# Optimization experiments

Measured on AMD Instinct MI355X. Metric: run time of the kernel, lower is better.

The kernel has to match this reference:

```python
import jax, jax.numpy as jnp
import numpy as np

V, D, F, M, N = 100000, 300, 768, 64, 512
SURF, CTX, DOC, BODY, H = 4, 50, 100, 200, 5


def setup_inputs() -> dict:
    key = jax.random.key(0)
    ks = jax.random.split(key, 24)
    f32 = jnp.float32
    inp = {
        'embed_table': jax.random.normal(ks[0], (V, D), f32) * 0.02,
        'W_ms': jax.random.normal(ks[1], (F, D, 2), f32) * 0.02,
        'b_ms': jnp.zeros((F,), f32),
        'W_mc': jax.random.normal(ks[2], (F, D, 5), f32) * 0.02,
        'b_mc': jnp.zeros((F,), f32),
        'att_W1': jax.random.normal(ks[3], (2 * D, D), f32) * 0.05,
        'att_b1': jnp.zeros((D,), f32),
        'att_W2': jax.random.normal(ks[4], (D, 1), f32) * 0.05,
        'att_b2': jnp.zeros((1,), f32),
        'll_W': jax.random.normal(ks[5], (7, 1), f32) * 0.3,
        'll_b': jnp.zeros((1,), f32),
        'lamda': jnp.asarray(0.5, f32),
        'mention_ids': jax.random.randint(ks[6], (M, SURF), 0, V, jnp.int32),
        'context_ids': jax.random.randint(ks[7], (M, CTX), 0, V, jnp.int32),
        'doc_ids': jax.random.randint(ks[8], (DOC,), 0, V, jnp.int32),
        'body_ids': jax.random.randint(ks[9], (N, BODY), 0, V, jnp.int32),
        'cand_ids': jax.random.randint(ks[10], (N,), 0, V, jnp.int32),
        'title_vec': jax.random.normal(ks[11], (N, F), f32),
        'bert_doc_vec': jax.random.normal(ks[12], (1, F), f32),
        'hand_features': jax.random.normal(ks[13], (N, 1), f32),
        'm2c_prior': jax.random.uniform(ks[14], (N,), f32),
        'mention_entity': jnp.ones((M, N), f32),
        'entity_entity': (jax.random.uniform(ks[15], (N, N)) < 0.2).astype(f32),
        'entity_sr': jax.random.uniform(ks[16], (N, N), f32),
        'random_k': 5,
    }
    return inp


def _conv_relu_avg(x, W, b):
    # x [B,L,300] -> conv1d(valid) -> relu -> mean over time -> [B,F]
    y = jax.lax.conv_general_dilated(jnp.transpose(x, (0, 2, 1)), W, (1,), 'VALID',
                                     dimension_numbers=('NCH', 'OIH', 'NCH'))
    return jax.nn.relu(y + b[None, :, None]).mean(axis=2)


def _l2n(x, eps=1e-6):
    return x / jnp.maximum(jnp.linalg.norm(x, axis=-1, keepdims=True), eps)


def reference(embed_table, W_ms, b_ms, W_mc, b_mc, att_W1, att_b1, att_W2, att_b2,
              ll_W, ll_b, lamda, mention_ids, context_ids, doc_ids, body_ids, cand_ids,
              title_vec, bert_doc_vec, hand_features, m2c_prior, mention_entity,
              entity_entity, entity_sr, random_k):
    d = embed_table.shape[1]
    hd = d // H
    men_emb = embed_table[mention_ids]           # [M,4,300]
    ctx_emb = embed_table[context_ids]           # [M,50,300]
    doc_emb = embed_table[doc_ids]               # [100,300]
    body_emb = embed_table[body_ids]             # [N,200,300]
    cand_emb = embed_table[cand_ids]             # [N,300]

    ms = _conv_relu_avg(men_emb, W_ms, b_ms)     # [M,768]
    mc = _conv_relu_avg(ctx_emb, W_mc, b_mc)     # [M,768]
    md = bert_doc_vec                            # [1,768]

    tn = _l2n(title_vec)
    cos_st = _l2n(ms) @ tn.T                     # [M,N]
    cos_dt = _l2n(md) @ tn.T                     # [1,N]
    cos_ct = _l2n(mc) @ tn.T                     # [M,N]

    # parameterless 5-head cross attention doc<->body, max over queries
    qh = doc_emb.reshape(doc_emb.shape[0], H, hd)
    kh = body_emb.reshape(body_emb.shape[0], body_emb.shape[1], H, hd)
    sc = jnp.einsum('qhd,nkhd->nhqk', qh, kh) / np.sqrt(hd).astype(np.float32)
    att_db = jnp.einsum('nhqk,nkhd->nqhd', jax.nn.softmax(sc, -1), kh)
    att_db = att_db.reshape(att_db.shape[0], att_db.shape[1], d).max(axis=1)   # [N,300]
    sc2 = jnp.einsum('nkhd,qhd->nhkq', kh, qh) / np.sqrt(hd).astype(np.float32)
    att_bd = jnp.einsum('nhkq,qhd->nkhd', jax.nn.softmax(sc2, -1), qh)
    att_bd = att_bd.reshape(att_bd.shape[0], att_bd.shape[1], d).max(axis=1)   # [N,300]
    comb = jnp.concatenate([att_db, att_bd], axis=-1)                          # [N,600]
    att_score = jax.nn.sigmoid(jax.nn.relu(comb @ att_W1 + att_b1) @ att_W2 + att_b2)[:, 0]  # [N]

    # local context attention ranker: max dot(cand, ctx token) / sqrt(d)
    local_att = jnp.einsum('itd,jd->ijt', ctx_emb, cand_emb).max(-1) / np.sqrt(d).astype(np.float32)  # [M,N]

    m, n = cos_st.shape
    feats = jnp.stack([
        jnp.broadcast_to(hand_features[:, 0][None, :], (m, n)),
        jnp.broadcast_to(m2c_prior[None, :], (m, n)),
        local_att,
        jnp.broadcast_to(att_score[None, :], (m, n)),
        cos_st,
        jnp.broadcast_to(cos_dt, (m, n)),
        cos_ct,
    ], axis=-1)                                   # [M,N,7]
    raw = jnp.einsum('mnf,fo->mn', feats, ll_W) + ll_b[0]

    mask = mention_entity
    cnt = mask.sum(1, keepdims=True)
    mean = (raw * mask).sum(1, keepdims=True) / cnt
    var = (((raw - mean) ** 2) * mask).sum(1, keepdims=True) / (cnt - 1)  # unbiased, torch.std
    z = (raw - mean) / jnp.sqrt(var)
    local_score = z * mask
    sm = jax.nn.softmax(jnp.where(mask > 0, z, -jnp.inf), axis=1) * mask
    zmin = jnp.min(jnp.where(mask > 0, z, jnp.inf), 1, keepdims=True)
    zmax = jnp.max(jnp.where(mask > 0, z, -jnp.inf), 1, keepdims=True)
    u = (z + 1 - zmin) / (zmax - zmin) * mask
    uni = u / u.sum(1, keepdims=True)

    # global score: keep top-3 candidates per mention, row-normalize SR, power-iterate
    top_idx = jax.lax.top_k(sm, 3)[1]                                   # [M,3]
    keep = jnp.zeros((n,), raw.dtype).at[top_idx.reshape(-1)].set(1.0)
    SR = entity_sr * entity_entity * keep[None, :]
    rs = SR.sum(1, keepdims=True)
    SR = jnp.where(jnp.abs(rs) < 1e-6, SR, SR / jnp.where(jnp.abs(rs) < 1e-6, 1.0, rs))
    s = sm.sum(0, keepdims=True)                                        # [1,N]
    fai = s
    for _ in range(int(random_k)):
        fai = (1 - lamda) * (fai @ SR) + lamda * s
    global_score = mention_entity * fai                                 # [M,N]
    return (s, fai, global_score)
```

## Files before the change

### kernel.cpp

```cpp
#include <hip/hip_runtime.h>
#include <math.h>

#define MM 64
#define NN 512
#define DD 300
#define FF 768
#define CTXL 50
#define DOCL 100
#define BODYL 200
#define NHEAD 5
#define HD 60

typedef __attribute__((ext_vector_type(8))) short bf16x8;
typedef __attribute__((ext_vector_type(4))) float f32x4;
#define MFMA16(A,B,C) __builtin_amdgcn_mfma_f32_16x16x32_bf16(A,B,C,0,0,0)

__device__ __forceinline__ ushort f2bf(float f) {
  uint u = __float_as_uint(f);
  uint r = (u + 0x7FFFu + ((u >> 16) & 1u)) >> 16;
  return (ushort)r;
}
__device__ __forceinline__ float bf2f(ushort h) {
  return __uint_as_float(((uint)h) << 16);
}

static constexpr size_t OFF_MS    = 0;
static constexpr size_t OFF_MC    = 49152;
static constexpr size_t OFF_TNORM = 98304;
static constexpr size_t OFF_COSDT = 98816;
static constexpr size_t OFF_CAND  = 99328;
static constexpr size_t OFF_DOC   = 252928;
static constexpr size_t OFF_COMB  = 282928;
static constexpr size_t OFF_ATTS  = 590128;
static constexpr size_t OFF_COSST = 590640;
static constexpr size_t OFF_COSCT = 623408;
static constexpr size_t OFF_LOCATT= 656176;
static constexpr size_t OFF_S     = 688944;
static constexpr size_t OFF_KEEP  = 689456;
static constexpr size_t OFF_INV   = 689968;
static constexpr size_t OFF_FAI_A = 690480;
static constexpr size_t OFF_FAI_B = 690992;
static constexpr size_t OFF_CTXG  = 691504;
static constexpr size_t OFF_WT    = 1689904;

__global__ __launch_bounds__(64) void k_init(
    const float* __restrict__ embed, const float* __restrict__ title,
    const float* __restrict__ bert, const int* __restrict__ cand_ids,
    const int* __restrict__ doc_ids, float* __restrict__ ws) {
  int n = blockIdx.x, t = threadIdx.x;
  float ss = 0.f, dd = 0.f, bb = 0.f;
  for (int j = t; j < FF; j += 64) {
    float tv = title[(size_t)n*FF + j], bv = bert[j];
    ss += tv*tv; dd += tv*bv; bb += bv*bv;
  }
#pragma unroll
  for (int o = 32; o; o >>= 1) {
    ss += __shfl_down(ss, o); dd += __shfl_down(dd, o); bb += __shfl_down(bb, o);
  }
  if (t == 0) {
    float tn = fmaxf(sqrtf(ss), 1e-6f);
    float bn = fmaxf(sqrtf(bb), 1e-6f);
    ws[OFF_TNORM + n] = tn;
    ws[OFF_COSDT + n] = dd / (tn * bn);
  }
  size_t cid = (size_t)cand_ids[n] * DD;
  for (int j = t; j < DD; j += 64) ws[OFF_CAND + (size_t)n*DD + j] = embed[cid + j];
  if (n < DOCL) {
    size_t did = (size_t)doc_ids[n] * DD;
    for (int j = t; j < DD; j += 64) ws[OFF_DOC + (size_t)n*DD + j] = embed[did + j];
  }
  if (n == 0) {
    for (int j = t; j < NN; j += 64) { ws[OFF_S + j] = 0.f; ws[OFF_KEEP + j] = 0.f; }
  }
}

__global__ __launch_bounds__(256) void k_gather(
    const float* __restrict__ embed, const int* __restrict__ context_ids,
    float* __restrict__ ws) {
  int m = blockIdx.x, t = threadIdx.x;
  float* dst = ws + OFF_CTXG + (size_t)m*52*DD;
  for (int i = t; i < 52*DD; i += 256) {
    int r = i / DD, c = i - r*DD;
    dst[i] = (r < CTXL) ? embed[(size_t)context_ids[m*CTXL + r]*DD + c] : 0.f;
  }
}

__global__ __launch_bounds__(256) void k_wt(
    const float* __restrict__ W, float* __restrict__ ws) {
  int kd = blockIdx.x;
  int k = kd / DD, d = kd - k*DD;
  int t = threadIdx.x;
  float* dst = ws + OFF_WT + (size_t)kd*FF;
  for (int f = t; f < FF; f += 256) dst[f] = W[(size_t)f*(DD*5) + d*5 + k];
}

__global__ __launch_bounds__(256) void k_ms(
    const float* __restrict__ embed, const int* __restrict__ mention_ids,
    const float* __restrict__ W, const float* __restrict__ b, float* __restrict__ ws) {
  __shared__ float x[4][DD];
  int m = blockIdx.x, t = threadIdx.x;
  for (int i = t; i < 4*DD; i += 256) {
    int r = i / DD, c = i % DD;
    x[r][c] = embed[(size_t)mention_ids[m*4 + r]*DD + c];
  }
  __syncthreads();
  for (int f = t; f < FF; f += 256) {
    const float* w = W + (size_t)f * (DD*2);
    float bb = b[f];
    float acc = 0.f;
#pragma unroll
    for (int tt = 0; tt < 3; ++tt) {
      float y = bb;
      for (int d = 0; d < DD; ++d) {
        float2 wv = *(const float2*)&w[d*2];
        y += wv.x * x[tt][d] + wv.y * x[tt+1][d];
      }
      acc += fmaxf(y, 0.f);
    }
    ws[OFF_MS + (size_t)m*FF + f] = acc * (1.f/3.f);
  }
}

__global__ __launch_bounds__(256) void k_mc_gemm(
    const float* __restrict__ b_mc, float* __restrict__ ws) {
  __shared__ float As[50][49];
  __shared__ float Bs[50][128];
  int m = blockIdx.x, f0 = blockIdx.y * 128, t = threadIdx.x;
  int tr = t >> 4, tc = t & 15;
  const float* ctxm = ws + OFF_CTXG + (size_t)m*52*DD;
  const float4* wt4 = (const float4*)(ws + OFF_WT);
  float acc[3][8];
#pragma unroll
  for (int r = 0; r < 3; ++r)
#pragma unroll
    for (int j = 0; j < 8; ++j) acc[r][j] = 0.f;

  for (int chunk = 0; chunk < 30; ++chunk) {
    int k = chunk / 6, dc = (chunk - k*6) * 50;
    for (int i = t; i < 48*50; i += 256) {
      int row = i / 50, kj = i - row*50;
      As[kj][row] = ctxm[(row + k)*DD + dc + kj];
    }
    for (int i = t; i < 1600; i += 256) {
      int kj = i >> 5, fq = i & 31;
      *(float4*)&Bs[kj][fq*4] = wt4[((size_t)(k*DD + dc + kj)*FF + f0 + fq*4) >> 2];
    }
    __syncthreads();
#pragma unroll 2
    for (int kj = 0; kj < 50; ++kj) {
      float a0 = As[kj][tr], a1 = As[kj][tr+16], a2 = As[kj][tr+32];
      float4 b0 = *(const float4*)&Bs[kj][tc*8];
      float4 b1 = *(const float4*)&Bs[kj][tc*8+4];
      float bb[8] = {b0.x,b0.y,b0.z,b0.w,b1.x,b1.y,b1.z,b1.w};
#pragma unroll
      for (int j = 0; j < 8; ++j) {
        acc[0][j] += a0*bb[j]; acc[1][j] += a1*bb[j]; acc[2][j] += a2*bb[j];
      }
    }
    __syncthreads();
  }
  float bv[8], p[8];
#pragma unroll
  for (int j = 0; j < 8; ++j) { bv[j] = b_mc[f0 + tc*8 + j]; p[j] = 0.f; }
#pragma unroll
  for (int rr = 0; rr < 3; ++rr) {
    int row = tr + 16*rr;
    if (row < 46) {
#pragma unroll
      for (int j = 0; j < 8; ++j) p[j] += fmaxf(acc[rr][j] + bv[j], 0.f);
    }
  }
  float* red = &Bs[0][0];
#pragma unroll
  for (int j = 0; j < 8; ++j) red[tr*128 + tc*8 + j] = p[j];
  __syncthreads();
  if (t < 128) {
    float s = 0.f;
#pragma unroll
    for (int i = 0; i < 16; ++i) s += red[i*128 + t];
    ws[OFF_MC + (size_t)m*FF + f0 + t] = s * (1.f/46.f);
  }
}

__global__ __launch_bounds__(256) void k_cos(
    const float* __restrict__ title, float* __restrict__ ws) {
  __shared__ float a[FF], bv_[FF];
  __shared__ float redA[4], redB[4];
  int m = blockIdx.x, t = threadIdx.x;
  float pa = 0.f, pb = 0.f;
  for (int j = t; j < FF; j += 256) {
    float v = ws[OFF_MS + (size_t)m*FF + j]; a[j] = v; pa += v*v;
    float u = ws[OFF_MC + (size_t)m*FF + j]; bv_[j] = u; pb += u*u;
  }
#pragma unroll
  for (int o = 32; o; o >>= 1) { pa += __shfl_down(pa, o); pb += __shfl_down(pb, o); }
  if ((t & 63) == 0) { redA[t>>6] = pa; redB[t>>6] = pb; }
  __syncthreads();
  float na = fmaxf(sqrtf(redA[0]+redA[1]+redA[2]+redA[3]), 1e-6f);
  float nb = fmaxf(sqrtf(redB[0]+redB[1]+redB[2]+redB[3]), 1e-6f);
  float ia = 1.f / na, ib = 1.f / nb;
  for (int n = t; n < NN; n += 256) {
    const float4* tr = (const float4*)(title + (size_t)n*FF);
    float ds = 0.f, dc = 0.f;
    for (int j = 0; j < FF/4; ++j) {
      float4 tv = tr[j];
      float4 av = *(const float4*)&a[j*4];
      float4 bw = *(const float4*)&bv_[j*4];
      ds += av.x*tv.x + av.y*tv.y + av.z*tv.z + av.w*tv.w;
      dc += bw.x*tv.x + bw.y*tv.y + bw.z*tv.z + bw.w*tv.w;
    }
    float it = 1.f / ws[OFF_TNORM + n];
    ws[OFF_COSST + (size_t)m*NN + n] = ds * ia * it;
    ws[OFF_COSCT + (size_t)m*NN + n] = dc * ib * it;
  }
}

__global__ __launch_bounds__(256) void k_att(
    const float* __restrict__ embed, const int* __restrict__ body_ids,
    float* __restrict__ ws) {
  __shared__ __align__(16) ushort qhB[112*64];
  __shared__ __align__(16) ushort qhT[64*128];
  __shared__ __align__(16) ushort khBc[32*64];
  __shared__ __align__(16) ushort khTc[64*48];
  __shared__ __align__(16) ushort XA[112*48];
  __shared__ __align__(16) ushort XT[32*128];
  __shared__ float rs_acc[112];
  __shared__ float cs_c[32];
  __shared__ float csqL[64];
  __shared__ float cskL[64];

  const float SCALE = 0.1290994448735806f;
  int n = blockIdx.x, h = blockIdx.y, t = threadIdx.x;
  int w = t >> 6, l = t & 63;
  int l15 = l & 15, l4 = l >> 4;
  const float* doc = ws + OFF_DOC;

  if (t < 112) rs_acc[t] = 0.f;
  else if (t < 176) cskL[t-112] = 0.f;
  if (t < 64) {
    int kk = t >> 1, ls = 14 + (t & 1);
    int ps = ls ^ (kk & 7);
    uint4 z = {0,0,0,0};
    *(uint4*)&XT[kk*128 + ps*8] = z;
  }

  for (int u = t; u < 112*8; u += 256) {
    int q = u >> 3, j8 = u & 7;
    uint pk[4] = {0,0,0,0};
    if (q < 100) {
      const float* src = doc + q*DD + h*HD;
#pragma unroll
      for (int i = 0; i < 8; ++i) {
        int j = j8*8 + i;
        float v = (j < HD) ? src[j] : 0.f;
        pk[i>>1] |= ((uint)f2bf(v)) << ((i & 1) * 16);
      }
    }
    int slot = j8 ^ (q & 7);
    *(uint4*)&qhB[q*64 + slot*8] = make_uint4(pk[0], pk[1], pk[2], pk[3]);
  }
  for (int u = t; u < 64*16; u += 256) {
    int d = u >> 4, q8 = u & 15;
    uint pk[4] = {0,0,0,0};
    if (d < HD) {
#pragma unroll
      for (int i = 0; i < 8; ++i) {
        int q = q8*8 + i;
        float v = (q < 100) ? doc[q*DD + h*HD + d] : 0.f;
        pk[i>>1] |= ((uint)f2bf(v)) << ((i & 1) * 16);
      }
    }
    int slot = q8 ^ (d & 7);
    *(uint4*)&qhT[d*128 + slot*8] = make_uint4(pk[0], pk[1], pk[2], pk[3]);
  }
  __syncthreads();
  if (t < 64) {
    int d = t;
    float s = 0.f;
    for (int ls = 0; ls < 13; ++ls) {
      int ps = ls ^ (d & 7);
      const ushort* p = &qhT[d*128 + ps*8];
#pragma unroll
      for (int i = 0; i < 8; ++i) {
        int q = ls*8 + i;
        if (q < 100) s += bf2f(p[i]);
      }
    }
    csqL[t] = s;
  }
  __syncthreads();
  float csq_r = csqL[16*w + l15];

  f32x4 Cdb[7];
#pragma unroll
  for (int i = 0; i < 7; ++i) Cdb[i] = (f32x4){0.f,0.f,0.f,0.f};
  float bdmx = -1e30f;

  const int* bids = body_ids + n*BODYL;

  for (int c = 0; c < 7; ++c) {
    int k0 = c * 32;
    {
      int kk = t >> 3, j8 = t & 7;
      int kg = k0 + kk;
      uint pk[4] = {0,0,0,0};
      if (kg < BODYL) {
        const float* src = embed + (size_t)bids[kg]*DD + h*HD;
#pragma unroll
        for (int i = 0; i < 8; ++i) {
          int j = j8*8 + i;
          float v = (j < HD) ? src[j] : 0.f;
          pk[i>>1] |= ((uint)f2bf(v)) << ((i & 1) * 16);
        }
      }
      int slot = j8 ^ (kk & 7);
      *(uint4*)&khBc[kk*64 + slot*8] = make_uint4(pk[0], pk[1], pk[2], pk[3]);
    }
    {
      int d = t >> 2, kk8 = t & 3;
      uint pk[4] = {0,0,0,0};
      if (d < HD) {
#pragma unroll
        for (int i = 0; i < 8; ++i) {
          int kg = k0 + kk8*8 + i;
          float v = (kg < BODYL) ? embed[(size_t)bids[kg]*DD + h*HD + d] : 0.f;
          pk[i>>1] |= ((uint)f2bf(v)) << ((i & 1) * 16);
        }
      }
      *(uint4*)&khTc[d*48 + kk8*8] = make_uint4(pk[0], pk[1], pk[2], pk[3]);
    }
    __syncthreads();

    for (int task = w; task < 14; task += 4) {
      int mt = task / 7, nt = task - mt*7;
      int krow = 16*mt + l15;
      int qrow = 16*nt + l15;
      f32x4 acc = {0.f,0.f,0.f,0.f};
#pragma unroll
      for (int js = 0; js < 2; ++js) {
        bf16x8 a = *(const bf16x8*)&khBc[krow*64 + ((js*4 + l4) ^ (krow & 7))*8];
        bf16x8 b = *(const bf16x8*)&qhB[qrow*64 + ((js*4 + l4) ^ (qrow & 7))*8];
        acc = MFMA16(a, b, acc);
      }
      int q = qrow;
      int kkb = 16*mt + 4*l4;
      ushort xs[4];
#pragma unroll
      for (int r = 0; r < 4; ++r) {
        int kg = k0 + kkb + r;
        float x = (q < 100 && kg < BODYL) ? (__expf(acc[r]*SCALE) - 1.f) : 0.f;
        xs[r] = f2bf(x);
      }
      uint2 wv = make_uint2((uint)xs[0] | ((uint)xs[1] << 16),
                            (uint)xs[2] | ((uint)xs[3] << 16));
      *(uint2*)&XA[q*48 + kkb] = wv;
#pragma unroll
      for (int r = 0; r < 4; ++r) {
        int kk = kkb + r;
        XT[kk*128 + (((q >> 3) ^ (kk & 7))*8) + (q & 7)] = xs[r];
      }
    }
    __syncthreads();

    if (t < 112) {
      float s = 0.f;
      const uint4* p = (const uint4*)&XA[t*48];
#pragma unroll
      for (int b4 = 0; b4 < 4; ++b4) {
        uint4 v = p[b4];
        uint vv[4] = {v.x, v.y, v.z, v.w};
#pragma unroll
        for (int i = 0; i < 4; ++i) {
          s += bf2f((ushort)(vv[i] & 0xFFFF)) + bf2f((ushort)(vv[i] >> 16));
        }
      }
      rs_acc[t] += s;
    } else if (t < 144) {
      int kk = t - 112;
      float s = 0.f;
      for (int ls = 0; ls < 14; ++ls) {
        int ps = ls ^ (kk & 7);
        const uint4* p = (const uint4*)&XT[kk*128 + ps*8];
        uint4 v = *p;
        uint vv[4] = {v.x, v.y, v.z, v.w};
#pragma unroll
        for (int i = 0; i < 4; ++i) {
          s += bf2f((ushort)(vv[i] & 0xFFFF)) + bf2f((ushort)(vv[i] >> 16));
        }
      }
      cs_c[kk] = 100.f + s;
    } else if (t < 208) {
      int d = t - 144;
      float s = 0.f;
      const uint4* p = (const uint4*)&khTc[d*48];
#pragma unroll
      for (int b4 = 0; b4 < 4; ++b4) {
        uint4 v = p[b4];
        uint vv[4] = {v.x, v.y, v.z, v.w};
#pragma unroll
        for (int i = 0; i < 4; ++i) {
          s += bf2f((ushort)(vv[i] & 0xFFFF)) + bf2f((ushort)(vv[i] >> 16));
        }
      }
      cskL[d] += s;
    }
    __syncthreads();

    {
      int d = 16*w + l15;
      bf16x8 bfr = *(const bf16x8*)&khTc[d*48 + l4*8];
#pragma unroll
      for (int mt2 = 0; mt2 < 7; ++mt2) {
        int q = 16*mt2 + l15;
        bf16x8 afr = *(const bf16x8*)&XA[q*48 + l4*8];
        Cdb[mt2] = MFMA16(afr, bfr, Cdb[mt2]);
      }
    }
    {
      int d = 16*w + l15;
#pragma unroll
      for (int kt = 0; kt < 2; ++kt) {
        int kk = 16*kt + l15;
        f32x4 acc3 = {0.f,0.f,0.f,0.f};
#pragma unroll
        for (int qs = 0; qs < 4; ++qs) {
          bf16x8 afr = *(const bf16x8*)&XT[kk*128 + ((qs*4 + l4) ^ (kk & 7))*8];
          bf16x8 bfr = *(const bf16x8*)&qhT[d*128 + ((qs*4 + l4) ^ (d & 7))*8];
          acc3 = MFMA16(afr, bfr, acc3);
        }
#pragma unroll
        for (int r = 0; r < 4; ++r) {
          int kkr = 16*kt + 4*l4 + r;
          int kg = k0 + kkr;
          if (kg < BODYL) {
            float v = (csq_r + acc3[r]) / cs_c[kkr];
            bdmx = fmaxf(bdmx, v);
          }
        }
      }
    }
    __syncthreads();
  }

  float csk_r = cskL[16*w + l15];
  float dbmx = -1e30f;
#pragma unroll
  for (int mt2 = 0; mt2 < 7; ++mt2) {
#pragma unroll
    for (int r = 0; r < 4; ++r) {
      int q = 16*mt2 + 4*l4 + r;
      if (q < 100) {
        float v = (csk_r + Cdb[mt2][r]) / (200.f + rs_acc[q]);
        dbmx = fmaxf(dbmx, v);
      }
    }
  }
  dbmx = fmaxf(dbmx, __shfl_xor(dbmx, 16));
  dbmx = fmaxf(dbmx, __shfl_xor(dbmx, 32));
  bdmx = fmaxf(bdmx, __shfl_xor(bdmx, 16));
  bdmx = fmaxf(bdmx, __shfl_xor(bdmx, 32));
  int d = 16*w + l15;
  if (l4 == 0 && d < HD) {
    ws[OFF_COMB + (size_t)n*600 + h*HD + d] = dbmx;
    ws[OFF_COMB + (size_t)n*600 + 300 + h*HD + d] = bdmx;
  }
}

__global__ __launch_bounds__(256) void k_local(
    float* __restrict__ ws) {
  __shared__ __align__(16) float x[CTXL][304];
  __shared__ float red[2][128];
  int m = blockIdx.x, nc = blockIdx.y, t = threadIdx.x;
  const float* ctxm = ws + OFF_CTXG + (size_t)m*52*DD;
  for (int i = t; i < CTXL*DD; i += 256) {
    int r = i / DD, c = i % DD;
    x[r][c] = ctxm[i];
  }
  __syncthreads();
  int nl = t & 127, half = t >> 7;
  int n = nc*128 + nl;
  const float4* cr = (const float4*)(ws + OFF_CAND + (size_t)n*DD);
  float acc[25];
#pragma unroll
  for (int i = 0; i < 25; ++i) acc[i] = 0.f;
  for (int d4 = 0; d4 < 75; ++d4) {
    float4 cv = cr[d4];
#pragma unroll
    for (int i = 0; i < 25; ++i) {
      float4 xv = *(const float4*)&x[half*25 + i][d4*4];
      acc[i] += xv.x*cv.x + xv.y*cv.y + xv.z*cv.z + xv.w*cv.w;
    }
  }
  float mx = -1e30f;
#pragma unroll
  for (int i = 0; i < 25; ++i) mx = fmaxf(mx, acc[i]);
  red[half][nl] = mx;
  __syncthreads();
  if (t < 128) {
    float v = fmaxf(red[0][t], red[1][t]) * 0.05773502691896258f;
    ws[OFF_LOCATT + (size_t)m*NN + nc*128 + t] = v;
  }
}

__global__ __launch_bounds__(256) void k_mlp(
    const float* __restrict__ W1, const float* __restrict__ b1,
    const float* __restrict__ W2, const float* __restrict__ b2,
    float* __restrict__ ws) {
  __shared__ float comb8[8][600];
  __shared__ float acc8[8];
  int b = blockIdx.x, t = threadIdx.x;
  int n0 = b*8;
  for (int i = t; i < 8*600; i += 256)
    comb8[i/600][i%600] = ws[OFF_COMB + (size_t)(n0 + i/600)*600 + (i%600)];
  if (t < 8) acc8[t] = 0.f;
  __syncthreads();
  float psum[8];
#pragma unroll
  for (int nn2 = 0; nn2 < 8; ++nn2) psum[nn2] = 0.f;
  for (int j = t; j < 300; j += 256) {
    float hh[8];
#pragma unroll
    for (int nn2 = 0; nn2 < 8; ++nn2) hh[nn2] = b1[j];
    for (int i = 0; i < 600; ++i) {
      float w = W1[(size_t)i*300 + j];
#pragma unroll
      for (int nn2 = 0; nn2 < 8; ++nn2) hh[nn2] += comb8[nn2][i]*w;
    }
    float w2 = W2[j];
#pragma unroll
    for (int nn2 = 0; nn2 < 8; ++nn2) psum[nn2] += fmaxf(hh[nn2], 0.f)*w2;
  }
#pragma unroll
  for (int nn2 = 0; nn2 < 8; ++nn2) atomicAdd(&acc8[nn2], psum[nn2]);
  __syncthreads();
  if (t < 8) {
    float v = acc8[t] + b2[0];
    ws[OFF_ATTS + n0 + t] = 1.f / (1.f + __expf(-v));
  }
}

__device__ __forceinline__ float bsum512(float v, float* red) {
  int t = threadIdx.x;
#pragma unroll
  for (int o = 32; o; o >>= 1) v += __shfl_down(v, o);
  __syncthreads();
  if ((t & 63) == 0) red[t>>6] = v;
  __syncthreads();
  float s = 0.f;
#pragma unroll
  for (int i = 0; i < 8; ++i) s += red[i];
  return s;
}
__device__ __forceinline__ float bmax512(float v, float* red) {
  int t = threadIdx.x;
#pragma unroll
  for (int o = 32; o; o >>= 1) v = fmaxf(v, __shfl_down(v, o));
  __syncthreads();
  if ((t & 63) == 0) red[t>>6] = v;
  __syncthreads();
  float s = -INFINITY;
#pragma unroll
  for (int i = 0; i < 8; ++i) s = fmaxf(s, red[i]);
  return s;
}

__global__ __launch_bounds__(512) void k_score(
    const float* __restrict__ hand, const float* __restrict__ m2c,
    const float* __restrict__ llW, const float* __restrict__ llb,
    const float* __restrict__ me, float* __restrict__ ws) {
  __shared__ float red[8];
  __shared__ float rv[512];
  __shared__ int ri[512];
  int m = blockIdx.x, t = threadIdx.x;
  float mask = me[(size_t)m*NN + t];
  float raw = llW[0]*hand[t] + llW[1]*m2c[t] + llW[2]*ws[OFF_LOCATT + (size_t)m*NN + t]
            + llW[3]*ws[OFF_ATTS + t] + llW[4]*ws[OFF_COSST + (size_t)m*NN + t]
            + llW[5]*ws[OFF_COSDT + t] + llW[6]*ws[OFF_COSCT + (size_t)m*NN + t] + llb[0];
  float cnt = bsum512(mask, red);
  float mean = bsum512(raw*mask, red) / cnt;
  float dv = raw - mean;
  float var = bsum512(dv*dv*mask, red) / (cnt - 1.f);
  float z = dv / sqrtf(var);
  float zm = (mask > 0.f) ? z : -INFINITY;
  float mx = bmax512(zm, red);
  float e = (mask > 0.f) ? __expf(zm - mx) : 0.f;
  float ssum = bsum512(e, red);
  float sm = e / ssum * mask;
  atomicAdd(&ws[OFF_S + t], sm);
  bool excl = false;
  for (int r = 0; r < 3; ++r) {
    rv[t] = excl ? -INFINITY : zm;
    ri[t] = t;
    __syncthreads();
    for (int off = 256; off; off >>= 1) {
      if (t < off) {
        float bb = rv[t+off]; int ib = ri[t+off];
        if (bb > rv[t] || (bb == rv[t] && ib < ri[t])) { rv[t] = bb; ri[t] = ib; }
      }
      __syncthreads();
    }
    int widx = ri[0];
    __syncthreads();
    if (t == 0) ws[OFF_KEEP + widx] = 1.f;
    if (t == widx) excl = true;
  }
}

__global__ __launch_bounds__(512) void k_grs(
    const float* __restrict__ esr, const float* __restrict__ eee,
    float* __restrict__ ws) {
  __shared__ float keep_l[NN];
  int b = blockIdx.x, t = threadIdx.x;
  keep_l[t] = ws[OFF_KEEP + t];
  __syncthreads();
  int lane = t & 63, w = t >> 6;
  int r = b*8 + w;
  float p = 0.f;
  for (int j = lane; j < NN; j += 64)
    p += esr[(size_t)r*NN + j] * eee[(size_t)r*NN + j] * keep_l[j];
#pragma unroll
  for (int o = 32; o; o >>= 1) p += __shfl_down(p, o);
  if (lane == 0) {
    ws[OFF_INV + r] = (fabsf(p) < 1e-6f) ? 1.f : 1.f/p;
    ws[OFF_FAI_A + r] = ws[OFF_S + r];
  }
}

__global__ __launch_bounds__(512) void k_giter(
    const float* __restrict__ esr, const float* __restrict__ eee,
    const float* __restrict__ lamda, const int* __restrict__ rk,
    const float* __restrict__ fin, float* __restrict__ fout,
    const float* __restrict__ wsro, int it) {
  int b = blockIdx.x, t = threadIdx.x;
  int K = rk[0];
  if (it >= K) {
    if (t < 8) fout[b*8 + t] = fin[b*8 + t];
    return;
  }
  __shared__ float g[NN];
  __shared__ float red[8][65];
  g[t] = fin[t] * wsro[OFF_INV + t];
  __syncthreads();
  float lam = lamda[0];
  int jl = t & 7, ig = t >> 3;
  int j = b*8 + jl;
  float p = 0.f;
  for (int i = ig; i < NN; i += 64)
    p += g[i] * esr[(size_t)i*NN + j] * eee[(size_t)i*NN + j];
  red[jl][ig] = p;
  __syncthreads();
  if (t < 8) {
    float acc = 0.f;
    for (int i = 0; i < 64; ++i) acc += red[t][i];
    int jj = b*8 + t;
    fout[jj] = (1.f - lam) * wsro[OFF_KEEP + jj] * acc + lam * wsro[OFF_S + jj];
  }
}

__global__ __launch_bounds__(512) void k_gout(
    const float* __restrict__ me, const float* __restrict__ ws, float* __restrict__ out) {
  int m = blockIdx.x, t = threadIdx.x;
  float fai = ws[OFF_FAI_A + t];
  if (m == 0) { out[t] = ws[OFF_S + t]; out[NN + t] = fai; }
  out[2*NN + (size_t)m*NN + t] = me[(size_t)m*NN + t] * fai;
}

extern "C" void kernel_launch(void* const* d_in, const int* in_sizes, int n_in,
                              void* d_out, int out_size, void* d_ws, size_t ws_size,
                              hipStream_t stream) {
  const float* embed   = (const float*)d_in[0];
  const float* W_ms    = (const float*)d_in[1];
  const float* b_ms    = (const float*)d_in[2];
  const float* W_mc    = (const float*)d_in[3];
  const float* b_mc    = (const float*)d_in[4];
  const float* att_W1  = (const float*)d_in[5];
  const float* att_b1  = (const float*)d_in[6];
  const float* att_W2  = (const float*)d_in[7];
  const float* att_b2  = (const float*)d_in[8];
  const float* ll_W    = (const float*)d_in[9];
  const float* ll_b    = (const float*)d_in[10];
  const float* lamda   = (const float*)d_in[11];
  const int* mention_ids = (const int*)d_in[12];
  const int* context_ids = (const int*)d_in[13];
  const int* doc_ids     = (const int*)d_in[14];
  const int* body_ids    = (const int*)d_in[15];
  const int* cand_ids    = (const int*)d_in[16];
  const float* title   = (const float*)d_in[17];
  const float* bert    = (const float*)d_in[18];
  const float* hand    = (const float*)d_in[19];
  const float* m2c     = (const float*)d_in[20];
  const float* me      = (const float*)d_in[21];
  const float* eee     = (const float*)d_in[22];
  const float* esr     = (const float*)d_in[23];
  const int* rk        = (const int*)d_in[24];
  float* ws  = (float*)d_ws;
  float* out = (float*)d_out;

  hipLaunchKernelGGL(k_init, dim3(NN), dim3(64), 0, stream, embed, title, bert, cand_ids, doc_ids, ws);
  hipLaunchKernelGGL(k_gather, dim3(MM), dim3(256), 0, stream, embed, context_ids, ws);
  hipLaunchKernelGGL(k_wt, dim3(1500), dim3(256), 0, stream, W_mc, ws);
  hipLaunchKernelGGL(k_ms, dim3(MM), dim3(256), 0, stream, embed, mention_ids, W_ms, b_ms, ws);
  hipLaunchKernelGGL(k_mc_gemm, dim3(MM, 6), dim3(256), 0, stream, b_mc, ws);
  hipLaunchKernelGGL(k_cos, dim3(MM), dim3(256), 0, stream, title, ws);
  hipLaunchKernelGGL(k_att, dim3(NN, NHEAD), dim3(256), 0, stream, embed, body_ids, ws);
  hipLaunchKernelGGL(k_local, dim3(MM, 4), dim3(256), 0, stream, ws);
  hipLaunchKernelGGL(k_mlp, dim3(64), dim3(256), 0, stream, att_W1, att_b1, att_W2, att_b2, ws);
  hipLaunchKernelGGL(k_score, dim3(MM), dim3(512), 0, stream, hand, m2c, ll_W, ll_b, me, ws);
  hipLaunchKernelGGL(k_grs, dim3(64), dim3(512), 0, stream, esr, eee, ws);
  float* fa = ws + OFF_FAI_A;
  float* fb = ws + OFF_FAI_B;
  for (int it = 0; it < 8; ++it) {
    hipLaunchKernelGGL(k_giter, dim3(64), dim3(512), 0, stream, esr, eee, lamda, rk,
                       (it & 1) ? fb : fa, (it & 1) ? fa : fb, ws, it);
  }
  hipLaunchKernelGGL(k_gout, dim3(MM), dim3(512), 0, stream, me, ws, out);
}
```

Measured before the change: 1.054 ms.

## Hoist doc bf16 prep, stage body in LDS once, MFMA sums, pretransposed SR

Doc head tiles are converted to bf16 once per head in a new kernel instead of in each of 2560 attention blocks. All 200 body rows now go into LDS up front, and row and column sums come from MFMA ones-columns instead of scalar reductions, which removes the per-chunk gather and the extra barrier. The normalized, keep-masked SR matrix is precomputed transposed so each power iteration reads one contiguous row per output. The mc GEMM tile also shrinks to 64 columns to launch more blocks. The cost is extra workspace and launches, plus a larger LDS footprint in the attention kernel that may lower occupancy.

Measured after the change: 994.7 us. 1.06x faster.

```diff
diff --git a/kernel.cpp b/kernel.cpp
--- a/kernel.cpp
+++ b/kernel.cpp
@@ -42,6 +42,10 @@
 static constexpr size_t OFF_FAI_B = 690992;
 static constexpr size_t OFF_CTXG  = 691504;
 static constexpr size_t OFF_WT    = 1689904;
+static constexpr size_t OFF_DOCB  = 2841904;
+static constexpr size_t OFF_DOCT  = 2859824;
+static constexpr size_t OFF_CSQ   = 2880304;
+static constexpr size_t OFF_SRNT  = 2880624;
 
 __global__ __launch_bounds__(64) void k_init(
     const float* __restrict__ embed, const float* __restrict__ title,
@@ -74,6 +78,46 @@
   }
 }
 
+__global__ __launch_bounds__(256) void k_doc(float* __restrict__ ws) {
+  int h = blockIdx.x, t = threadIdx.x;
+  const float* doc = ws + OFF_DOC;
+  ushort* docB = (ushort*)(ws + OFF_DOCB) + h*112*64;
+  ushort* docT = (ushort*)(ws + OFF_DOCT) + h*64*128;
+  for (int u = t; u < 112*8; u += 256) {
+    int q = u >> 3, j8 = u & 7;
+    uint pk[4] = {0,0,0,0};
+    if (q < DOCL) {
+#pragma unroll
+      for (int i = 0; i < 8; ++i) {
+        int j = j8*8 + i;
+        float v = (j < HD) ? doc[q*DD + h*HD + j] : 0.f;
+        pk[i>>1] |= ((uint)f2bf(v)) << ((i & 1) * 16);
+      }
+    }
+    *(uint4*)&docB[q*64 + j8*8] = make_uint4(pk[0],pk[1],pk[2],pk[3]);
+  }
+  for (int u = t; u < 64*16; u += 256) {
+    int d = u >> 4, q8 = u & 15;
+    uint pk[4] = {0,0,0,0};
+#pragma unroll
+    for (int i = 0; i < 8; ++i) {
+      int q = q8*8 + i;
+      float v = 0.f;
+      if (q < DOCL) {
+        if (d < HD) v = doc[q*DD + h*HD + d];
+        else if (d == HD) v = 1.f;
+      }
+      pk[i>>1] |= ((uint)f2bf(v)) << ((i & 1) * 16);
+    }
+    *(uint4*)&docT[d*128 + q8*8] = make_uint4(pk[0],pk[1],pk[2],pk[3]);
+  }
+  if (t < 64) {
+    float s = 0.f;
+    if (t < HD) for (int q = 0; q < DOCL; ++q) s += bf2f(f2bf(doc[q*DD + h*HD + t]));
+    ws[OFF_CSQ + h*64 + t] = s;
+  }
+}
+
 __global__ __launch_bounds__(256) void k_gather(
     const float* __restrict__ embed, const int* __restrict__ context_ids,
     float* __restrict__ ws) {
@@ -124,16 +168,16 @@
 __global__ __launch_bounds__(256) void k_mc_gemm(
     const float* __restrict__ b_mc, float* __restrict__ ws) {
   __shared__ float As[50][49];
-  __shared__ float Bs[50][128];
-  int m = blockIdx.x, f0 = blockIdx.y * 128, t = threadIdx.x;
+  __shared__ float Bs[50][64];
+  int m = blockIdx.x, f0 = blockIdx.y * 64, t = threadIdx.x;
   int tr = t >> 4, tc = t & 15;
   const float* ctxm = ws + OFF_CTXG + (size_t)m*52*DD;
   const float4* wt4 = (const float4*)(ws + OFF_WT);
-  float acc[3][8];
+  float acc[3][4];
 #pragma unroll
   for (int r = 0; r < 3; ++r)
 #pragma unroll
-    for (int j = 0; j < 8; ++j) acc[r][j] = 0.f;
+    for (int j = 0; j < 4; ++j) acc[r][j] = 0.f;
 
   for (int chunk = 0; chunk < 30; ++chunk) {
     int k = chunk / 6, dc = (chunk - k*6) * 50;
@@ -141,43 +185,42 @@
       int row = i / 50, kj = i - row*50;
       As[kj][row] = ctxm[(row + k)*DD + dc + kj];
     }
-    for (int i = t; i < 1600; i += 256) {
-      int kj = i >> 5, fq = i & 31;
+    for (int i = t; i < 800; i += 256) {
+      int kj = i >> 4, fq = i & 15;
       *(float4*)&Bs[kj][fq*4] = wt4[((size_t)(k*DD + dc + kj)*FF + f0 + fq*4) >> 2];
     }
     __syncthreads();
 #pragma unroll 2
     for (int kj = 0; kj < 50; ++kj) {
       float a0 = As[kj][tr], a1 = As[kj][tr+16], a2 = As[kj][tr+32];
-      float4 b0 = *(const float4*)&Bs[kj][tc*8];
-      float4 b1 = *(const float4*)&Bs[kj][tc*8+4];
-      float bb[8] = {b0.x,b0.y,b0.z,b0.w,b1.x,b1.y,b1.z,b1.w};
-#pragma unroll
-      for (int j = 0; j < 8; ++j) {
+      float4 b0 = *(const float4*)&Bs[kj][tc*4];
+      float bb[4] = {b0.x,b0.y,b0.z,b0.w};
+#pragma unroll
+      for (int j = 0; j < 4; ++j) {
         acc[0][j] += a0*bb[j]; acc[1][j] += a1*bb[j]; acc[2][j] += a2*bb[j];
       }
     }
     __syncthreads();
   }
-  float bv[8], p[8];
-#pragma unroll
-  for (int j = 0; j < 8; ++j) { bv[j] = b_mc[f0 + tc*8 + j]; p[j] = 0.f; }
+  float bv[4], p[4];
+#pragma unroll
+  for (int j = 0; j < 4; ++j) { bv[j] = b_mc[f0 + tc*4 + j]; p[j] = 0.f; }
 #pragma unroll
   for (int rr = 0; rr < 3; ++rr) {
     int row = tr + 16*rr;
     if (row < 46) {
 #pragma unroll
-      for (int j = 0; j < 8; ++j) p[j] += fmaxf(acc[rr][j] + bv[j], 0.f);
-    }
-  }
-  float* red = &Bs[0][0];
-#pragma unroll
-  for (int j = 0; j < 8; ++j) red[tr*128 + tc*8 + j] = p[j];
-  __syncthreads();
-  if (t < 128) {
+      for (int j = 0; j < 4; ++j) p[j] += fmaxf(acc[rr][j] + bv[j], 0.f);
+    }
+  }
+  float* red = &As[0][0];
+#pragma unroll
+  for (int j = 0; j < 4; ++j) red[tr*64 + tc*4 + j] = p[j];
+  __syncthreads();
+  if (t < 64) {
     float s = 0.f;
 #pragma unroll
-    for (int i = 0; i < 16; ++i) s += red[i*128 + t];
+    for (int i = 0; i < 16; ++i) s += red[i*64 + t];
     ws[OFF_MC + (size_t)m*FF + f0 + t] = s * (1.f/46.f);
   }
 }
@@ -218,239 +261,168 @@
 __global__ __launch_bounds__(256) void k_att(
     const float* __restrict__ embed, const int* __restrict__ body_ids,
     float* __restrict__ ws) {
-  __shared__ __align__(16) ushort qhB[112*64];
-  __shared__ __align__(16) ushort qhT[64*128];
-  __shared__ __align__(16) ushort khBc[32*64];
-  __shared__ __align__(16) ushort khTc[64*48];
-  __shared__ __align__(16) ushort XA[112*48];
+  __shared__ __align__(16) ushort khB[224*64];
+  __shared__ __align__(16) ushort khT[64*232];
+  __shared__ __align__(16) ushort XA[112*56];
   __shared__ __align__(16) ushort XT[32*128];
-  __shared__ float rs_acc[112];
+  __shared__ float rs_l[112];
   __shared__ float cs_c[32];
-  __shared__ float csqL[64];
-  __shared__ float cskL[64];
 
   const float SCALE = 0.1290994448735806f;
   int n = blockIdx.x, h = blockIdx.y, t = threadIdx.x;
   int w = t >> 6, l = t & 63;
   int l15 = l & 15, l4 = l >> 4;
-  const float* doc = ws + OFF_DOC;
-
-  if (t < 112) rs_acc[t] = 0.f;
-  else if (t < 176) cskL[t-112] = 0.f;
-  if (t < 64) {
-    int kk = t >> 1, ls = 14 + (t & 1);
-    int ps = ls ^ (kk & 7);
-    uint4 z = {0,0,0,0};
-    *(uint4*)&XT[kk*128 + ps*8] = z;
-  }
-
-  for (int u = t; u < 112*8; u += 256) {
-    int q = u >> 3, j8 = u & 7;
+  const int* bids = body_ids + n*BODYL;
+  const ushort* docB = (const ushort*)(ws + OFF_DOCB) + h*112*64;
+  const ushort* docT = (const ushort*)(ws + OFF_DOCT) + h*64*128;
+  int dcol = 16*w + l15;
+  float csq_r = ws[OFF_CSQ + h*64 + dcol];
+
+  for (int u = t; u < 224*8; u += 256) {
+    int k = u >> 3, j8 = u & 7;
     uint pk[4] = {0,0,0,0};
-    if (q < 100) {
-      const float* src = doc + q*DD + h*HD;
-#pragma unroll
-      for (int i = 0; i < 8; ++i) {
-        int j = j8*8 + i;
-        float v = (j < HD) ? src[j] : 0.f;
-        pk[i>>1] |= ((uint)f2bf(v)) << ((i & 1) * 16);
-      }
-    }
-    int slot = j8 ^ (q & 7);
-    *(uint4*)&qhB[q*64 + slot*8] = make_uint4(pk[0], pk[1], pk[2], pk[3]);
-  }
-  for (int u = t; u < 64*16; u += 256) {
-    int d = u >> 4, q8 = u & 15;
-    uint pk[4] = {0,0,0,0};
-    if (d < HD) {
-#pragma unroll
-      for (int i = 0; i < 8; ++i) {
-        int q = q8*8 + i;
-        float v = (q < 100) ? doc[q*DD + h*HD + d] : 0.f;
-        pk[i>>1] |= ((uint)f2bf(v)) << ((i & 1) * 16);
-      }
-    }
-    int slot = q8 ^ (d & 7);
-    *(uint4*)&qhT[d*128 + slot*8] = make_uint4(pk[0], pk[1], pk[2], pk[3]);
-  }
-  __syncthreads();
-  if (t < 64) {
-    int d = t;
-    float s = 0.f;
-    for (int ls = 0; ls < 13; ++ls) {
-      int ps = ls ^ (d & 7);
-      const ushort* p = &qhT[d*128 + ps*8];
-#pragma unroll
-      for (int i = 0; i < 8; ++i) {
-        int q = ls*8 + i;
-        if (q < 100) s += bf2f(p[i]);
-      }
-    }
-    csqL[t] = s;
-  }
-  __syncthreads();
-  float csq_r = csqL[16*w + l15];
+    if (k < BODYL) {
+      const float* src = embed + (size_t)bids[k]*DD + h*HD;
+      float4 v0 = *(const float4*)&src[j8*8];
+      float4 v1 = {0.f,0.f,0.f,0.f};
+      if (j8 < 7) v1 = *(const float4*)&src[j8*8+4];
+      pk[0] = (uint)f2bf(v0.x) | ((uint)f2bf(v0.y) << 16);
+      pk[1] = (uint)f2bf(v0.z) | ((uint)f2bf(v0.w) << 16);
+      pk[2] = (uint)f2bf(v1.x) | ((uint)f2bf(v1.y) << 16);
+      pk[3] = (uint)f2bf(v1.z) | ((uint)f2bf(v1.w) << 16);
+    }
+    *(uint4*)&khB[k*64 + (j8 ^ (k & 7))*8] = make_uint4(pk[0],pk[1],pk[2],pk[3]);
+  }
+  for (int u = t; u < 512; u += 256) {
+    int kk = u >> 4, q = 112 + (u & 15);
+    XT[kk*128 + ((q >> 3) ^ (kk & 7))*8 + (q & 7)] = 0;
+  }
+  __syncthreads();
+  for (int v = t; v < 232*64; v += 256) {
+    int d = v & 63, k = v >> 6;
+    ushort val = 0;
+    if (k < BODYL) {
+      if (d < HD) val = khB[k*64 + ((d >> 3) ^ (k & 7))*8 + (d & 7)];
+      else if (d == HD) val = 0x3F80;
+    }
+    khT[d*232 + k] = val;
+  }
+  __syncthreads();
 
   f32x4 Cdb[7];
 #pragma unroll
   for (int i = 0; i < 7; ++i) Cdb[i] = (f32x4){0.f,0.f,0.f,0.f};
-  float bdmx = -1e30f;
-
-  const int* bids = body_ids + n*BODYL;
+  float bdmx = -1e30f, dbmx = -1e30f;
+
+  bf16x8 bfrT[4];
+#pragma unroll
+  for (int qs = 0; qs < 4; ++qs)
+    bfrT[qs] = *(const bf16x8*)&docT[dcol*128 + qs*32 + l4*8];
 
   for (int c = 0; c < 7; ++c) {
-    int k0 = c * 32;
+    int k0 = c*32;
+    for (int task = w; task < 14; task += 4) {
+      int mt = (task >= 7) ? 1 : 0;
+      int nt = task - mt*7;
+      int krow = k0 + 16*mt + l15;
+      int qrow = 16*nt + l15;
+      bf16x8 ka0 = *(const bf16x8*)&khB[krow*64 + ((0 + l4) ^ (krow & 7))*8];
+      bf16x8 ka1 = *(const bf16x8*)&khB[krow*64 + ((4 + l4) ^ (krow & 7))*8];
+      bf16x8 qa0 = *(const bf16x8*)&docB[qrow*64 + l4*8];
+      bf16x8 qa1 = *(const bf16x8*)&docB[qrow*64 + 32 + l4*8];
+      f32x4 d1 = (f32x4){0.f,0.f,0.f,0.f}, d1b = (f32x4){0.f,0.f,0.f,0.f};
+      d1  = MFMA16(ka0, qa0, d1);  d1  = MFMA16(ka1, qa1, d1);
+      d1b = MFMA16(qa0, ka0, d1b); d1b = MFMA16(qa1, ka1, d1b);
+      {
+        int kkb = 16*mt + 4*l4;
+        ushort xs[4];
+#pragma unroll
+        for (int r = 0; r < 4; ++r) {
+          int kg = k0 + kkb + r;
+          float x = 0.f;
+          if (qrow < DOCL) { if (kg < BODYL) x = __expf(d1[r]*SCALE) - 1.f; }
+          else if (qrow == DOCL) { if (kg < BODYL) x = 1.f; }
+          xs[r] = f2bf(x);
+        }
+        uint2 wv = make_uint2((uint)xs[0] | ((uint)xs[1] << 16),
+                              (uint)xs[2] | ((uint)xs[3] << 16));
+        *(uint2*)&XA[qrow*56 + kkb] = wv;
+      }
+      {
+        int kk = 16*mt + l15;
+        int kg = k0 + kk;
+        int q0 = 16*nt + 4*l4;
+        ushort xs[4];
+#pragma unroll
+        for (int r = 0; r < 4; ++r) {
+          int q = q0 + r;
+          float x = (q < DOCL && kg < BODYL) ? (__expf(d1b[r]*SCALE) - 1.f) : 0.f;
+          xs[r] = f2bf(x);
+        }
+        uint2 wv = make_uint2((uint)xs[0] | ((uint)xs[1] << 16),
+                              (uint)xs[2] | ((uint)xs[3] << 16));
+        *(uint2*)&XT[kk*128 + ((q0 >> 3) ^ (kk & 7))*8 + (q0 & 7)] = wv;
+      }
+    }
+    __syncthreads();
     {
-      int kk = t >> 3, j8 = t & 7;
-      int kg = k0 + kk;
-      uint pk[4] = {0,0,0,0};
-      if (kg < BODYL) {
-        const float* src = embed + (size_t)bids[kg]*DD + h*HD;
-#pragma unroll
-        for (int i = 0; i < 8; ++i) {
-          int j = j8*8 + i;
-          float v = (j < HD) ? src[j] : 0.f;
-          pk[i>>1] |= ((uint)f2bf(v)) << ((i & 1) * 16);
+      bf16x8 bfr = *(const bf16x8*)&khT[dcol*232 + k0 + l4*8];
+#pragma unroll
+      for (int mt2 = 0; mt2 < 7; ++mt2) {
+        bf16x8 afr = *(const bf16x8*)&XA[(16*mt2 + l15)*56 + l4*8];
+        Cdb[mt2] = MFMA16(afr, bfr, Cdb[mt2]);
+      }
+    }
+    f32x4 a3[2];
+#pragma unroll
+    for (int kt = 0; kt < 2; ++kt) {
+      int kkl = 16*kt + l15;
+      f32x4 acc = (f32x4){0.f,0.f,0.f,0.f};
+#pragma unroll
+      for (int qs = 0; qs < 4; ++qs) {
+        bf16x8 afr = *(const bf16x8*)&XT[kkl*128 + ((qs*4 + l4) ^ (kkl & 7))*8];
+        acc = MFMA16(afr, bfrT[qs], acc);
+      }
+      a3[kt] = acc;
+    }
+    if (w == 3 && l15 == 12) {
+#pragma unroll
+      for (int kt = 0; kt < 2; ++kt)
+#pragma unroll
+        for (int r = 0; r < 4; ++r)
+          cs_c[16*kt + 4*l4 + r] = 100.f + a3[kt][r];
+    }
+    __syncthreads();
+#pragma unroll
+    for (int kt = 0; kt < 2; ++kt) {
+#pragma unroll
+      for (int r = 0; r < 4; ++r) {
+        int kk = 16*kt + 4*l4 + r;
+        if (k0 + kk < BODYL) {
+          float v = (csq_r + a3[kt][r]) / cs_c[kk];
+          bdmx = fmaxf(bdmx, v);
         }
       }
-      int slot = j8 ^ (kk & 7);
-      *(uint4*)&khBc[kk*64 + slot*8] = make_uint4(pk[0], pk[1], pk[2], pk[3]);
-    }
-    {
-      int d = t >> 2, kk8 = t & 3;
-      uint pk[4] = {0,0,0,0};
-      if (d < HD) {
-#pragma unroll
-        for (int i = 0; i < 8; ++i) {
-          int kg = k0 + kk8*8 + i;
-          float v = (kg < BODYL) ? embed[(size_t)bids[kg]*DD + h*HD + d] : 0.f;
-          pk[i>>1] |= ((uint)f2bf(v)) << ((i & 1) * 16);
-        }
-      }
-      *(uint4*)&khTc[d*48 + kk8*8] = make_uint4(pk[0], pk[1], pk[2], pk[3]);
     }
     __syncthreads();
-
-    for (int task = w; task < 14; task += 4) {
-      int mt = task / 7, nt = task - mt*7;
-      int krow = 16*mt + l15;
-      int qrow = 16*nt + l15;
-      f32x4 acc = {0.f,0.f,0.f,0.f};
-#pragma unroll
-      for (int js = 0; js < 2; ++js) {
-        bf16x8 a = *(const bf16x8*)&khBc[krow*64 + ((js*4 + l4) ^ (krow & 7))*8];
-        bf16x8 b = *(const bf16x8*)&qhB[qrow*64 + ((js*4 + l4) ^ (qrow & 7))*8];
-        acc = MFMA16(a, b, acc);
-      }
-      int q = qrow;
-      int kkb = 16*mt + 4*l4;
-      ushort xs[4];
-#pragma unroll
-      for (int r = 0; r < 4; ++r) {
-        int kg = k0 + kkb + r;
-        float x = (q < 100 && kg < BODYL) ? (__expf(acc[r]*SCALE) - 1.f) : 0.f;
-        xs[r] = f2bf(x);
-      }
-      uint2 wv = make_uint2((uint)xs[0] | ((uint)xs[1] << 16),
-                            (uint)xs[2] | ((uint)xs[3] << 16));
-      *(uint2*)&XA[q*48 + kkb] = wv;
-#pragma unroll
-      for (int r = 0; r < 4; ++r) {
-        int kk = kkb + r;
-        XT[kk*128 + (((q >> 3) ^ (kk & 7))*8) + (q & 7)] = xs[r];
-      }
-    }
-    __syncthreads();
-
-    if (t < 112) {
-      float s = 0.f;
-      const uint4* p = (const uint4*)&XA[t*48];
-#pragma unroll
-      for (int b4 = 0; b4 < 4; ++b4) {
-        uint4 v = p[b4];
-        uint vv[4] = {v.x, v.y, v.z, v.w};
-#pragma unroll
-        for (int i = 0; i < 4; ++i) {
-          s += bf2f((ushort)(vv[i] & 0xFFFF)) + bf2f((ushort)(vv[i] >> 16));
-        }
-      }
-      rs_acc[t] += s;
-    } else if (t < 144) {
-      int kk = t - 112;
-      float s = 0.f;
-      for (int ls = 0; ls < 14; ++ls) {
-        int ps = ls ^ (kk & 7);
-        const uint4* p = (const uint4*)&XT[kk*128 + ps*8];
-        uint4 v = *p;
-        uint vv[4] = {v.x, v.y, v.z, v.w};
-#pragma unroll
-        for (int i = 0; i < 4; ++i) {
-          s += bf2f((ushort)(vv[i] & 0xFFFF)) + bf2f((ushort)(vv[i] >> 16));
-        }
-      }
-      cs_c[kk] = 100.f + s;
-    } else if (t < 208) {
-      int d = t - 144;
-      float s = 0.f;
-      const uint4* p = (const uint4*)&khTc[d*48];
-#pragma unroll
-      for (int b4 = 0; b4 < 4; ++b4) {
-        uint4 v = p[b4];
-        uint vv[4] = {v.x, v.y, v.z, v.w};
-#pragma unroll
-        for (int i = 0; i < 4; ++i) {
-          s += bf2f((ushort)(vv[i] & 0xFFFF)) + bf2f((ushort)(vv[i] >> 16));
-        }
-      }
-      cskL[d] += s;
-    }
-    __syncthreads();
-
-    {
-      int d = 16*w + l15;
-      bf16x8 bfr = *(const bf16x8*)&khTc[d*48 + l4*8];
-#pragma unroll
-      for (int mt2 = 0; mt2 < 7; ++mt2) {
-        int q = 16*mt2 + l15;
-        bf16x8 afr = *(const bf16x8*)&XA[q*48 + l4*8];
-        Cdb[mt2] = MFMA16(afr, bfr, Cdb[mt2]);
-      }
-    }
-    {
-      int d = 16*w + l15;
-#pragma unroll
-      for (int kt = 0; kt < 2; ++kt) {
-        int kk = 16*kt + l15;
-        f32x4 acc3 = {0.f,0.f,0.f,0.f};
-#pragma unroll
-        for (int qs = 0; qs < 4; ++qs) {
-          bf16x8 afr = *(const bf16x8*)&XT[kk*128 + ((qs*4 + l4) ^ (kk & 7))*8];
-          bf16x8 bfr = *(const bf16x8*)&qhT[d*128 + ((qs*4 + l4) ^ (d & 7))*8];
-          acc3 = MFMA16(afr, bfr, acc3);
-        }
-#pragma unroll
-        for (int r = 0; r < 4; ++r) {
-          int kkr = 16*kt + 4*l4 + r;
-          int kg = k0 + kkr;
-          if (kg < BODYL) {
-            float v = (csq_r + acc3[r]) / cs_c[kkr];
-            bdmx = fmaxf(bdmx, v);
-          }
-        }
-      }
-    }
-    __syncthreads();
-  }
-
-  float csk_r = cskL[16*w + l15];
-  float dbmx = -1e30f;
+  }
+
+  if (w == 3 && l15 == 12) {
+#pragma unroll
+    for (int mt2 = 0; mt2 < 7; ++mt2)
+#pragma unroll
+      for (int r = 0; r < 4; ++r)
+        rs_l[16*mt2 + 4*l4 + r] = Cdb[mt2][r];
+  }
+  float csk_r = __shfl(Cdb[6][0], 16 + l15);
+  __syncthreads();
 #pragma unroll
   for (int mt2 = 0; mt2 < 7; ++mt2) {
 #pragma unroll
     for (int r = 0; r < 4; ++r) {
       int q = 16*mt2 + 4*l4 + r;
-      if (q < 100) {
-        float v = (csk_r + Cdb[mt2][r]) / (200.f + rs_acc[q]);
+      if (q < DOCL) {
+        float v = (csk_r + Cdb[mt2][r]) / (200.f + rs_l[q]);
         dbmx = fmaxf(dbmx, v);
       }
     }
@@ -459,10 +431,9 @@
   dbmx = fmaxf(dbmx, __shfl_xor(dbmx, 32));
   bdmx = fmaxf(bdmx, __shfl_xor(bdmx, 16));
   bdmx = fmaxf(bdmx, __shfl_xor(bdmx, 32));
-  int d = 16*w + l15;
-  if (l4 == 0 && d < HD) {
-    ws[OFF_COMB + (size_t)n*600 + h*HD + d] = dbmx;
-    ws[OFF_COMB + (size_t)n*600 + 300 + h*HD + d] = bdmx;
+  if (l4 == 0 && dcol < HD) {
+    ws[OFF_COMB + (size_t)n*600 + h*HD + dcol] = dbmx;
+    ws[OFF_COMB + (size_t)n*600 + 300 + h*HD + dcol] = bdmx;
   }
 }
 
@@ -626,34 +597,32 @@
   }
 }
 
-__global__ __launch_bounds__(512) void k_giter(
+__global__ __launch_bounds__(256) void k_srt(
     const float* __restrict__ esr, const float* __restrict__ eee,
+    float* __restrict__ ws) {
+  int j = blockIdx.x, t = threadIdx.x;
+  float kj = ws[OFF_KEEP + j];
+  float* dst = ws + OFF_SRNT + (size_t)j*NN;
+  for (int i = t; i < NN; i += 256)
+    dst[i] = esr[(size_t)i*NN + j] * eee[(size_t)i*NN + j] * kj * ws[OFF_INV + i];
+}
+
+__global__ __launch_bounds__(256) void k_giter(
     const float* __restrict__ lamda, const int* __restrict__ rk,
     const float* __restrict__ fin, float* __restrict__ fout,
     const float* __restrict__ wsro, int it) {
-  int b = blockIdx.x, t = threadIdx.x;
-  int K = rk[0];
-  if (it >= K) {
-    if (t < 8) fout[b*8 + t] = fin[b*8 + t];
-    return;
-  }
-  __shared__ float g[NN];
-  __shared__ float red[8][65];
-  g[t] = fin[t] * wsro[OFF_INV + t];
-  __syncthreads();
-  float lam = lamda[0];
-  int jl = t & 7, ig = t >> 3;
-  int j = b*8 + jl;
-  float p = 0.f;
-  for (int i = ig; i < NN; i += 64)
-    p += g[i] * esr[(size_t)i*NN + j] * eee[(size_t)i*NN + j];
-  red[jl][ig] = p;
-  __syncthreads();
-  if (t < 8) {
-    float acc = 0.f;
-    for (int i = 0; i < 64; ++i) acc += red[t][i];
-    int jj = b*8 + t;
-    fout[jj] = (1.f - lam) * wsro[OFF_KEEP + jj] * acc + lam * wsro[OFF_S + jj];
+  int j = blockIdx.x, t = threadIdx.x;
+  if (it >= rk[0]) { if (t == 0) fout[j] = fin[j]; return; }
+  __shared__ float red[4];
+  const float* srn = wsro + OFF_SRNT + (size_t)j*NN;
+  float p = fin[t]*srn[t] + fin[t+256]*srn[t+256];
+#pragma unroll
+  for (int o = 32; o; o >>= 1) p += __shfl_down(p, o);
+  if ((t & 63) == 0) red[t>>6] = p;
+  __syncthreads();
+  if (t == 0) {
+    float lam = lamda[0];
+    fout[j] = (1.f - lam)*(red[0]+red[1]+red[2]+red[3]) + lam*wsro[OFF_S + j];
   }
 }
 
@@ -697,20 +666,22 @@
   float* out = (float*)d_out;
 
   hipLaunchKernelGGL(k_init, dim3(NN), dim3(64), 0, stream, embed, title, bert, cand_ids, doc_ids, ws);
+  hipLaunchKernelGGL(k_doc, dim3(NHEAD), dim3(256), 0, stream, ws);
   hipLaunchKernelGGL(k_gather, dim3(MM), dim3(256), 0, stream, embed, context_ids, ws);
   hipLaunchKernelGGL(k_wt, dim3(1500), dim3(256), 0, stream, W_mc, ws);
   hipLaunchKernelGGL(k_ms, dim3(MM), dim3(256), 0, stream, embed, mention_ids, W_ms, b_ms, ws);
-  hipLaunchKernelGGL(k_mc_gemm, dim3(MM, 6), dim3(256), 0, stream, b_mc, ws);
+  hipLaunchKernelGGL(k_mc_gemm, dim3(MM, 12), dim3(256), 0, stream, b_mc, ws);
   hipLaunchKernelGGL(k_cos, dim3(MM), dim3(256), 0, stream, title, ws);
   hipLaunchKernelGGL(k_att, dim3(NN, NHEAD), dim3(256), 0, stream, embed, body_ids, ws);
   hipLaunchKernelGGL(k_local, dim3(MM, 4), dim3(256), 0, stream, ws);
   hipLaunchKernelGGL(k_mlp, dim3(64), dim3(256), 0, stream, att_W1, att_b1, att_W2, att_b2, ws);
   hipLaunchKernelGGL(k_score, dim3(MM), dim3(512), 0, stream, hand, m2c, ll_W, ll_b, me, ws);
   hipLaunchKernelGGL(k_grs, dim3(64), dim3(512), 0, stream, esr, eee, ws);
+  hipLaunchKernelGGL(k_srt, dim3(NN), dim3(256), 0, stream, esr, eee, ws);
   float* fa = ws + OFF_FAI_A;
   float* fb = ws + OFF_FAI_B;
   for (int it = 0; it < 8; ++it) {
-    hipLaunchKernelGGL(k_giter, dim3(64), dim3(512), 0, stream, esr, eee, lamda, rk,
+    hipLaunchKernelGGL(k_giter, dim3(NN), dim3(256), 0, stream, lamda, rk,
                        (it & 1) ? fb : fa, (it & 1) ? fa : fb, ws, it);
   }
   hipLaunchKernelGGL(k_gout, dim3(MM), dim3(512), 0, stream, me, ws, out);
```
